# Optimization experiments

Measured on AMD Instinct MI355X. Metric: run time of the kernel, lower is better.

Reference implementation:

```python
import jax, jax.numpy as jnp
import numpy as np

DIM = 1024
HEADS = 16
DIM_HEAD = 64
SEG = 512           # segment_len (+ 0 longterm mem tokens)
PMEM = 16           # num_persist_mem_tokens
THETA = 10000.0
RMS_EPS = 1.1920929e-07  # torch.finfo(float32).eps (nn.RMSNorm default eps=None)


def setup_inputs() -> dict:
    key = jax.random.key(0)
    k0, k1, k2, k3 = jax.random.split(key, 4)
    dim_inner = HEADS * DIM_HEAD
    seq = jax.random.normal(k0, (2, 4096, DIM), jnp.float32)
    norm_w = jnp.ones((DIM,), jnp.float32)
    w_qkv = jax.random.normal(k1, (DIM, 3 * dim_inner), jnp.float32) * (DIM ** -0.5)
    w_out = jax.random.normal(k2, (dim_inner, DIM), jnp.float32) * (dim_inner ** -0.5)
    # nn.Parameter is zeros at init; use small random values for a meaningful test
    pmem = jax.random.normal(k3, (2, HEADS, PMEM, DIM_HEAD), jnp.float32) * 0.02
    return {"seq": seq, "norm_w": norm_w, "w_qkv": w_qkv, "w_out": w_out, "pmem": pmem}


def _rope(x):
    # interleaved (pairwise) rotary over the full head dim, positions 0..n-1 per segment
    n, d = x.shape[-2], x.shape[-1]
    inv_freq = 1.0 / (THETA ** (jnp.arange(0, d, 2, dtype=jnp.float32) / d))
    freqs = jnp.arange(n, dtype=jnp.float32)[:, None] * inv_freq[None, :]  # (n, d/2)
    freqs = jnp.repeat(freqs, 2, axis=-1)                                  # (n, d)
    cos, sin = jnp.cos(freqs), jnp.sin(freqs)
    x1, x2 = x[..., 0::2], x[..., 1::2]
    x_rot = jnp.stack((-x2, x1), axis=-1).reshape(x.shape)
    return x * cos + x_rot * sin


def reference(seq, norm_w, w_qkv, w_out, pmem):
    b, s, d = seq.shape
    w = s // SEG  # seq_len is an exact multiple of segment_len (no pad branch)
    x = seq.reshape(b * w, SEG, d)  # 'b (w n) d -> (b w) n d'
    # RMSNorm
    x = x * jax.lax.rsqrt(jnp.mean(x * x, axis=-1, keepdims=True) + RMS_EPS) * norm_w
    q, k, v = jnp.split(x @ w_qkv, 3, axis=-1)
    sh = lambda t: t.reshape(b * w, SEG, HEADS, DIM_HEAD).transpose(0, 2, 1, 3)  # b n (h d) -> b h n d
    q, k, v = sh(q), sh(k), sh(v)
    orig_v = v
    q, k = _rope(q), _rope(k)
    pmk = jnp.broadcast_to(pmem[0], (b * w, HEADS, PMEM, DIM_HEAD))
    pmv = jnp.broadcast_to(pmem[1], (b * w, HEADS, PMEM, DIM_HEAD))
    k = jnp.concatenate((pmk, k), axis=-2)  # (bw, h, PMEM+SEG, dh)
    v = jnp.concatenate((pmv, v), axis=-2)
    scores = jnp.einsum('bhid,bhjd->bhij', q, k) * (DIM_HEAD ** -0.5)
    i = jnp.arange(SEG)[:, None]
    j = jnp.arange(SEG + PMEM)[None, :]
    mask = (j < PMEM) | ((j - PMEM) <= i)  # persist tokens always visible; causal within segment
    scores = jnp.where(mask, scores, -1e30)
    attn = jax.nn.softmax(scores, axis=-1)
    out = jnp.einsum('bhij,bhjd->bhid', attn, v)
    out = out.transpose(0, 2, 1, 3).reshape(b * w, SEG, HEADS * DIM_HEAD)  # merge heads
    out = (out @ w_out).reshape(b, s, d)  # inverse_segment (no pad to trim)
    return out, orig_v
```

## Files before the change

### kernel.cpp

```cpp
#include <hip/hip_runtime.h>
#include <hip/hip_bf16.h>

#define DIM    1024
#define HEADS  16
#define DH     64
#define SEG    512
#define PMEMN  16
#define TOK    8192
#define NQKV   3072
#define JPAD   544
#define NSH    256
#define VTS    129
#define QKS    136
#define VFS    132

typedef __hip_bfloat16 bf16;
typedef __attribute__((ext_vector_type(8))) short short8;
typedef __attribute__((ext_vector_type(4))) float floatx4;

__device__ __forceinline__ short8 ld_frag(const bf16* p) {
    return *(const short8*)p;
}
__device__ __forceinline__ floatx4 mfma16(short8 a, short8 b, floatx4 c) {
    return __builtin_amdgcn_mfma_f32_16x16x32_bf16(a, b, c, 0, 0, 0);
}
__device__ __forceinline__ void g2lds16(const bf16* g, bf16* l) {
    __builtin_amdgcn_global_load_lds((const __attribute__((address_space(1))) void*)g,
                                     (__attribute__((address_space(3))) void*)l, 16, 0, 0);
}

__global__ void rmsnorm_kernel(const float* __restrict__ x, const float* __restrict__ wgt,
                               bf16* __restrict__ xn) {
    int row = blockIdx.x;
    int tid = threadIdx.x;
    const float4* xr = (const float4*)(x + (long)row * DIM);
    float4 v = xr[tid];
    float ss = v.x * v.x + v.y * v.y + v.z * v.z + v.w * v.w;
    #pragma unroll
    for (int off = 32; off; off >>= 1) ss += __shfl_xor(ss, off);
    __shared__ float red[4];
    if ((tid & 63) == 0) red[tid >> 6] = ss;
    __syncthreads();
    float tot = red[0] + red[1] + red[2] + red[3];
    float sc = rsqrtf(tot * (1.0f / DIM) + 1.1920929e-07f);
    const float4* wr = (const float4*)wgt;
    float4 w4 = wr[tid];
    bf16* o = xn + (long)row * DIM + tid * 4;
    o[0] = __float2bfloat16(v.x * sc * w4.x);
    o[1] = __float2bfloat16(v.y * sc * w4.y);
    o[2] = __float2bfloat16(v.z * sc * w4.z);
    o[3] = __float2bfloat16(v.w * sc * w4.w);
}

__global__ void transpose_w2(const float* __restrict__ wqkv, const float* __restrict__ wout,
                             bf16* __restrict__ wqkvT, bf16* __restrict__ woutT) {
    __shared__ float tile[32][33];
    int bx = blockIdx.x;
    const float* in; bf16* out; int C, c0;
    if (bx < 96) { in = wqkv; out = wqkvT; C = NQKV; c0 = bx * 32; }
    else         { in = wout; out = woutT; C = DIM;  c0 = (bx - 96) * 32; }
    const int R = DIM;
    int r0 = blockIdx.y * 32;
    int tx = threadIdx.x, ty = threadIdx.y;
    #pragma unroll
    for (int i = 0; i < 4; i++)
        tile[ty + i * 8][tx] = in[(long)(r0 + ty + i * 8) * C + c0 + tx];
    __syncthreads();
    #pragma unroll
    for (int i = 0; i < 4; i++)
        out[(long)(c0 + ty + i * 8) * R + r0 + tx] = __float2bfloat16(tile[tx][ty + i * 8]);
}

__global__ __launch_bounds__(256)
void gemm_bt_f(const bf16* __restrict__ A, const bf16* __restrict__ Bt,
               float* __restrict__ C, int M, int N, int K) {
    __shared__ __align__(16) bf16 SMu[128 * 136];
    bf16* As = SMu;
    bf16* Bs = SMu + 128 * 64;
    const int tid = threadIdx.x;
    const int wv = tid >> 6;
    const int lane = tid & 63;
    const int quad = lane >> 4, l15 = lane & 15;
    const int wm = (wv >> 1) * 64, wn = (wv & 1) * 64;
    const int bm = blockIdx.x, bn = blockIdx.y;

    const int srow = tid >> 3;
    const int sgch = (tid & 7) ^ (srow & 7);
    const bf16* Ag = A + (long)(bm * 128 + srow) * K + sgch * 8;
    const bf16* Bg = Bt + (long)(bn * 128 + srow) * K + sgch * 8;
    const long row32 = (long)32 * K;

    const int rx0 = ((0 + quad) ^ (l15 & 7)) * 8;
    const int rx1 = ((4 + quad) ^ (l15 & 7)) * 8;

    floatx4 acc[4][4] = {};

    for (int k0 = 0; k0 < K; k0 += 64) {
        __syncthreads();
        #pragma unroll
        for (int i = 0; i < 4; i++) {
            g2lds16(Ag + i * row32 + k0, As + i * 2048 + tid * 8);
            g2lds16(Bg + i * row32 + k0, Bs + i * 2048 + tid * 8);
        }
        __syncthreads();
        #pragma unroll
        for (int kk = 0; kk < 2; kk++) {
            const int rx = kk ? rx1 : rx0;
            short8 af[4], bfr[4];
            #pragma unroll
            for (int i = 0; i < 4; i++) af[i] = ld_frag(&As[(wm + i * 16 + l15) * 64 + rx]);
            #pragma unroll
            for (int j = 0; j < 4; j++) bfr[j] = ld_frag(&Bs[(wn + j * 16 + l15) * 64 + rx]);
            #pragma unroll
            for (int i = 0; i < 4; i++)
                #pragma unroll
                for (int j = 0; j < 4; j++)
                    acc[i][j] = mfma16(af[i], bfr[j], acc[i][j]);
        }
    }
    float* SMf = (float*)SMu;
    #pragma unroll
    for (int half = 0; half < 2; half++) {
        __syncthreads();
        if ((wv >> 1) == half) {
            #pragma unroll
            for (int i = 0; i < 4; i++)
                #pragma unroll
                for (int j = 0; j < 4; j++)
                    #pragma unroll
                    for (int r = 0; r < 4; r++)
                        SMf[(i * 16 + quad * 4 + r) * VFS + wn + j * 16 + l15] = acc[i][j][r];
        }
        __syncthreads();
        #pragma unroll
        for (int it = 0; it < 8; it++) {
            int cid = it * 256 + tid;
            int rr = cid >> 5, cc = cid & 31;
            float4 v4 = *(const float4*)&SMf[rr * VFS + cc * 4];
            *(float4*)&C[(long)(bm * 128 + half * 64 + rr) * N + bn * 128 + cc * 4] = v4;
        }
    }
}

__global__ __launch_bounds__(256)
void gemm_qkv_ep(const bf16* __restrict__ A, const bf16* __restrict__ Bt,
                 bf16* __restrict__ qbuf, bf16* __restrict__ kpad,
                 bf16* __restrict__ vtpad, float* __restrict__ origv) {
    const int K = DIM, N = NQKV;
    __shared__ __align__(16) bf16 SM[128 * 136];
    bf16* As = SM;
    bf16* Bs = SM + 128 * 64;
    const int tid = threadIdx.x;
    const int wv = tid >> 6;
    const int lane = tid & 63;
    const int quad = lane >> 4, l15 = lane & 15;
    const int wm = (wv >> 1) * 64, wn = (wv & 1) * 64;
    const int bm = blockIdx.x, bn = blockIdx.y;

    const int strow = tid >> 3;
    const int sgch = (tid & 7) ^ (strow & 7);
    const bf16* Ag = A + (long)(bm * 128 + strow) * K + sgch * 8;
    const bf16* Bg = Bt + (long)(bn * 128 + strow) * K + sgch * 8;
    const long row32 = (long)32 * K;

    const int rx0 = ((0 + quad) ^ (l15 & 7)) * 8;
    const int rx1 = ((4 + quad) ^ (l15 & 7)) * 8;

    floatx4 acc[4][4] = {};

    for (int k0 = 0; k0 < K; k0 += 64) {
        __syncthreads();
        #pragma unroll
        for (int i = 0; i < 4; i++) {
            g2lds16(Ag + i * row32 + k0, As + i * 2048 + tid * 8);
            g2lds16(Bg + i * row32 + k0, Bs + i * 2048 + tid * 8);
        }
        __syncthreads();
        #pragma unroll
        for (int kk = 0; kk < 2; kk++) {
            const int rx = kk ? rx1 : rx0;
            short8 af[4], bfr[4];
            #pragma unroll
            for (int i = 0; i < 4; i++) af[i] = ld_frag(&As[(wm + i * 16 + l15) * 64 + rx]);
            #pragma unroll
            for (int j = 0; j < 4; j++) bfr[j] = ld_frag(&Bs[(wn + j * 16 + l15) * 64 + rx]);
            #pragma unroll
            for (int i = 0; i < 4; i++)
                #pragma unroll
                for (int j = 0; j < 4; j++)
                    acc[i][j] = mfma16(af[i], bfr[j], acc[i][j]);
        }
    }

    const int tok0 = bm * 128;
    const int seg = tok0 >> 9;
    const int s0 = tok0 & 511;

    if (bn < 16) {
        const bool isq = (bn < 8);
        __syncthreads();
        #pragma unroll
        for (int j = 0; j < 4; j++) {
            int col = wn + j * 16 + l15;
            int dcol = (bn * 128 + col) & 1023;
            int dh = dcol & 63;
            int pr = dh >> 1;
            float invf = __expf(-(float)pr * (9.210340371976184f / 32.0f));
            const bool odd = dh & 1;
            #pragma unroll
            for (int i = 0; i < 4; i++)
                #pragma unroll
                for (int r = 0; r < 4; r++) {
                    int sl = s0 + wm + i * 16 + quad * 4 + r;
                    float sn, cs;
                    __sincosf((float)sl * invf, &sn, &cs);
                    float v = acc[i][j][r];
                    float px = __shfl_xor(v, 1);
                    float y = odd ? (v * cs + px * sn) : (v * cs - px * sn);
                    if (isq) y *= 0.125f;
                    SM[(wm + i * 16 + quad * 4 + r) * QKS + col] = __float2bfloat16(y);
                }
        }
        __syncthreads();
        #pragma unroll
        for (int it = 0; it < 8; it++) {
            int cid = it * 256 + tid;
            int rr = cid >> 4, cc = cid & 15;
            short8 pk = *(const short8*)&SM[rr * QKS + cc * 8];
            if (isq) {
                *(short8*)&qbuf[(long)(tok0 + rr) * DIM + bn * 128 + cc * 8] = pk;
            } else {
                int lc = cc * 8;
                int h = ((bn - 8) * 128 + lc) >> 6;
                int dh = lc & 63;
                *(short8*)&kpad[(((long)(seg * 16 + h) * JPAD) + PMEMN + s0 + rr) * DH + dh] = pk;
            }
        }
    } else {
        const int vq = bn - 16;
        const int h0 = vq * 2;
        float* SMf = (float*)SM;
        #pragma unroll
        for (int half = 0; half < 2; half++) {
            __syncthreads();
            if ((wv >> 1) == half) {
                #pragma unroll
                for (int i = 0; i < 4; i++)
                    #pragma unroll
                    for (int j = 0; j < 4; j++)
                        #pragma unroll
                        for (int r = 0; r < 4; r++)
                            SMf[(i * 16 + quad * 4 + r) * VFS + wn + j * 16 + l15] = acc[i][j][r];
            }
            __syncthreads();
            #pragma unroll
            for (int it = 0; it < 8; it++) {
                int cid = it * 256 + tid;
                int rr = cid >> 5, cc = cid & 31;
                int h = h0 + (cc >> 4), dh = (cc * 4) & 63;
                float4 v4 = *(const float4*)&SMf[rr * VFS + cc * 4];
                int sl = s0 + half * 64 + rr;
                *(float4*)&origv[((long)(seg * 16 + h) * SEG + sl) * DH + dh] = v4;
            }
        }
        __syncthreads();
        #pragma unroll
        for (int i = 0; i < 4; i++)
            #pragma unroll
            for (int j = 0; j < 4; j++)
                #pragma unroll
                for (int r = 0; r < 4; r++)
                    SM[(wm + i * 16 + quad * 4 + r) * VTS + wn + j * 16 + l15] =
                        __float2bfloat16(acc[i][j][r]);
        __syncthreads();
        #pragma unroll
        for (int it = 0; it < 8; it++) {
            int cid = it * 256 + tid;
            int orow = cid >> 4;
            int tch = cid & 15;
            int vcol = vq * 128 + orow;
            int h = vcol >> 6, dh = vcol & 63;
            short8 pk;
            #pragma unroll
            for (int k = 0; k < 8; k++) {
                bf16 t = SM[(tch * 8 + k) * VTS + orow];
                pk[k] = __builtin_bit_cast(short, t);
            }
            *(short8*)&vtpad[(((long)(seg * 16 + h) * DH + dh) * JPAD) + PMEMN + s0 + tch * 8] = pk;
        }
    }
}

__global__ void fill_pmem_pad(const float* __restrict__ pmem, bf16* __restrict__ kpad,
                              bf16* __restrict__ vtpad) {
    int gid = blockIdx.x * 256 + threadIdx.x;
    int dh = gid & 63, j = (gid >> 6) & 15, sh = gid >> 10;
    int h = sh & 15;
    float kv = pmem[((0 * HEADS + h) * PMEMN + j) * DH + dh];
    float vv = pmem[((1 * HEADS + h) * PMEMN + j) * DH + dh];
    kpad[((long)sh * JPAD + j) * DH + dh] = __float2bfloat16(kv);
    vtpad[((long)sh * DH + dh) * JPAD + j] = __float2bfloat16(vv);
    kpad[((long)sh * JPAD + PMEMN + SEG + j) * DH + dh] = __float2bfloat16(0.0f);
    vtpad[((long)sh * DH + dh) * JPAD + PMEMN + SEG + j] = __float2bfloat16(0.0f);
}

__global__ __launch_bounds__(256, 3)
void flash_attn(const bf16* __restrict__ qbuf, const bf16* __restrict__ kpad,
                const bf16* __restrict__ vtpad, bf16* __restrict__ attn_out) {
    const int bid = blockIdx.x;
    const int sh = bid & (NSH - 1);
    const int qblk = bid >> 8;
    const int wv = threadIdx.x >> 6;
    const int lane = threadIdx.x & 63;
    const int quad = lane >> 4, l15 = lane & 15;
    const int qr0 = qblk * 128 + wv * 32;
    const int bw = sh >> 4, h = sh & 15;

    __shared__ __align__(16) short pbuf[4][32 * 32];
    short* pb = pbuf[wv];

    const bf16* qr_g0 = qbuf + (long)(bw * SEG + qr0 + l15) * DIM + h * DH;
    const bf16* qr_g1 = qbuf + (long)(bw * SEG + qr0 + 16 + l15) * DIM + h * DH;
    short8 aq[2][2] = {{ld_frag(qr_g0 + quad * 8), ld_frag(qr_g0 + 32 + quad * 8)},
                       {ld_frag(qr_g1 + quad * 8), ld_frag(qr_g1 + 32 + quad * 8)}};

    const short bf16one = (short)0x3F80;
    short8 onesB;
    #pragma unroll
    for (int i = 0; i < 8; i++) onesB[i] = (l15 == 0) ? bf16one : (short)0;

    float mrow[2][4];
    floatx4 o[2][4] = {};
    floatx4 lac[2] = {};
    #pragma unroll
    for (int g = 0; g < 2; g++)
        #pragma unroll
        for (int r = 0; r < 4; r++) mrow[g][r] = -1e30f;

    const bf16* kb = kpad + (long)sh * JPAD * DH;
    const bf16* vbp = vtpad + (long)sh * DH * JPAD;

    const int ntiles = (qr0 + 47) / 32 + 1;

    short8 kf[4];
    {
        const bf16* kr0 = kb + (long)l15 * DH;
        const bf16* kr1 = kb + (long)(16 + l15) * DH;
        kf[0] = ld_frag(kr0 + quad * 8);  kf[1] = ld_frag(kr0 + 32 + quad * 8);
        kf[2] = ld_frag(kr1 + quad * 8);  kf[3] = ld_frag(kr1 + 32 + quad * 8);
    }

    for (int jt = 0; jt < ntiles; ++jt) {
        const int j0 = jt * 32;
        short8 bv[4];
        #pragma unroll
        for (int n = 0; n < 4; n++)
            bv[n] = ld_frag(vbp + (long)(n * 16 + l15) * JPAD + j0 + quad * 8);

        floatx4 sc[2][2];
        #pragma unroll
        for (int g = 0; g < 2; g++) {
            sc[g][0] = mfma16(aq[g][1], kf[1], mfma16(aq[g][0], kf[0], floatx4{}));
            sc[g][1] = mfma16(aq[g][1], kf[3], mfma16(aq[g][0], kf[2], floatx4{}));
        }
        {
            const int jn = (jt + 1 < ntiles) ? j0 + 32 : j0;
            const bf16* kr0 = kb + (long)(jn + l15) * DH;
            const bf16* kr1 = kb + (long)(jn + 16 + l15) * DH;
            kf[0] = ld_frag(kr0 + quad * 8);  kf[1] = ld_frag(kr0 + 32 + quad * 8);
            kf[2] = ld_frag(kr1 + quad * 8);  kf[3] = ld_frag(kr1 + 32 + quad * 8);
        }

        float alpha[2][4];
        #pragma unroll
        for (int g = 0; g < 2; g++) {
            #pragma unroll
            for (int r = 0; r < 4; r++) {
                int qi = qr0 + g * 16 + quad * 4 + r;
                int ja = j0 + l15;
                int jb = j0 + 16 + l15;
                float va  = ((ja < PMEMN) || (ja - PMEMN <= qi)) ? sc[g][0][r] : -1e30f;
                float vb2 = ((jb < PMEMN) || (jb - PMEMN <= qi)) ? sc[g][1][r] : -1e30f;
                float rm = fmaxf(va, vb2);
                #pragma unroll
                for (int off = 1; off < 16; off <<= 1) rm = fmaxf(rm, __shfl_xor(rm, off));
                float mn = fmaxf(mrow[g][r], rm);
                alpha[g][r] = __expf(mrow[g][r] - mn);
                mrow[g][r] = mn;
                float p0 = __expf(va - mn);
                float p1 = __expf(vb2 - mn);
                pb[(g * 16 + quad * 4 + r) * 32 + l15]      = __builtin_bit_cast(short, __float2bfloat16(p0));
                pb[(g * 16 + quad * 4 + r) * 32 + 16 + l15] = __builtin_bit_cast(short, __float2bfloat16(p1));
            }
        }
        __asm__ volatile("" ::: "memory");
        short8 pa0, pa1;
        __builtin_memcpy(&pa0, &pb[l15 * 32 + quad * 8], 16);
        __builtin_memcpy(&pa1, &pb[(16 + l15) * 32 + quad * 8], 16);
        __asm__ volatile("" ::: "memory");
        #pragma unroll
        for (int r = 0; r < 4; r++) { lac[0][r] *= alpha[0][r]; lac[1][r] *= alpha[1][r]; }
        lac[0] = mfma16(pa0, onesB, lac[0]);
        lac[1] = mfma16(pa1, onesB, lac[1]);
        #pragma unroll
        for (int n = 0; n < 4; n++) {
            #pragma unroll
            for (int r = 0; r < 4; r++) { o[0][n][r] *= alpha[0][r]; o[1][n][r] *= alpha[1][r]; }
            o[0][n] = mfma16(pa0, bv[n], o[0][n]);
            o[1][n] = mfma16(pa1, bv[n], o[1][n]);
        }
    }
    #pragma unroll
    for (int g = 0; g < 2; g++) {
        bf16* orow = attn_out + (long)(bw * SEG + qr0 + g * 16 + quad * 4) * DIM + h * DH;
        #pragma unroll
        for (int r = 0; r < 4; r++) {
            float lsum = __shfl(lac[g][r], (lane & 48));
            float inv = 1.0f / lsum;
            #pragma unroll
            for (int n = 0; n < 4; n++)
                orow[(long)r * DIM + n * 16 + l15] = __float2bfloat16(o[g][n][r] * inv);
        }
    }
}

extern "C" void kernel_launch(void* const* d_in, const int* in_sizes, int n_in,
                              void* d_out, int out_size, void* d_ws, size_t ws_size,
                              hipStream_t stream) {
    const float* seq    = (const float*)d_in[0];
    const float* norm_w = (const float*)d_in[1];
    const float* w_qkv  = (const float*)d_in[2];
    const float* w_out  = (const float*)d_in[3];
    const float* pmem   = (const float*)d_in[4];
    float* out   = (float*)d_out;
    float* origv = out + (long)TOK * DIM;

    char* p = (char*)d_ws;
    bf16* xn     = (bf16*)p; p += (long)TOK * DIM * 2;
    bf16* wqkvT  = (bf16*)p; p += (long)NQKV * DIM * 2;
    bf16* woutT  = (bf16*)p; p += (long)DIM * DIM * 2;
    bf16* qbuf   = (bf16*)p; p += (long)TOK * DIM * 2;
    bf16* kpadb  = (bf16*)p; p += (long)NSH * JPAD * DH * 2;
    bf16* vtpadb = (bf16*)p; p += (long)NSH * DH * JPAD * 2;
    bf16* attno  = xn;

    rmsnorm_kernel<<<TOK, 256, 0, stream>>>(seq, norm_w, xn);
    transpose_w2<<<dim3(128, 32), dim3(32, 8), 0, stream>>>(w_qkv, w_out, wqkvT, woutT);
    fill_pmem_pad<<<(NSH * PMEMN * DH) / 256, 256, 0, stream>>>(pmem, kpadb, vtpadb);
    gemm_qkv_ep<<<dim3(TOK / 128, NQKV / 128), 256, 0, stream>>>(xn, wqkvT, qbuf, kpadb, vtpadb, origv);
    flash_attn<<<4 * NSH, 256, 0, stream>>>(qbuf, kpadb, vtpadb, attno);
    gemm_bt_f<<<dim3(TOK / 128, DIM / 128), 256, 0, stream>>>(attno, woutT, out, TOK, DIM, DIM);
}
```

Before: 241.6 us.

## Rewrite QKV GEMM as 256x256 tile, 8-wave, double-buffered pipelined kernel

```diff
diff --git a/kernel.cpp b/kernel.cpp
--- a/kernel.cpp
+++ b/kernel.cpp
@@ -11,8 +11,9 @@
 #define JPAD   544
 #define NSH    256
 #define VTS    129
-#define QKS    136
-#define VFS    132
+#define QK2    264
+#define VF2    260
+#define VT2    257
 
 typedef __hip_bfloat16 bf16;
 typedef __attribute__((ext_vector_type(8))) short short8;
@@ -24,6 +25,8 @@
 __device__ __forceinline__ floatx4 mfma16(short8 a, short8 b, floatx4 c) {
     return __builtin_amdgcn_mfma_f32_16x16x32_bf16(a, b, c, 0, 0, 0);
 }
+__device__ __forceinline__ void st_out(bf16* p, float v) { *p = __float2bfloat16(v); }
+__device__ __forceinline__ void st_out(float* p, float v) { *p = v; }
 __device__ __forceinline__ void g2lds16(const bf16* g, bf16* l) {
     __builtin_amdgcn_global_load_lds((const __attribute__((address_space(1))) void*)g,
                                      (__attribute__((address_space(3))) void*)l, 16, 0, 0);
@@ -129,164 +132,210 @@
                 for (int j = 0; j < 4; j++)
                     #pragma unroll
                     for (int r = 0; r < 4; r++)
-                        SMf[(i * 16 + quad * 4 + r) * VFS + wn + j * 16 + l15] = acc[i][j][r];
+                        SMf[(i * 16 + quad * 4 + r) * 132 + wn + j * 16 + l15] = acc[i][j][r];
         }
         __syncthreads();
         #pragma unroll
         for (int it = 0; it < 8; it++) {
             int cid = it * 256 + tid;
             int rr = cid >> 5, cc = cid & 31;
-            float4 v4 = *(const float4*)&SMf[rr * VFS + cc * 4];
+            float4 v4 = *(const float4*)&SMf[rr * 132 + cc * 4];
             *(float4*)&C[(long)(bm * 128 + half * 64 + rr) * N + bn * 128 + cc * 4] = v4;
         }
     }
 }
 
-__global__ __launch_bounds__(256)
+__global__ __launch_bounds__(512, 2)
 void gemm_qkv_ep(const bf16* __restrict__ A, const bf16* __restrict__ Bt,
                  bf16* __restrict__ qbuf, bf16* __restrict__ kpad,
                  bf16* __restrict__ vtpad, float* __restrict__ origv) {
-    const int K = DIM, N = NQKV;
-    __shared__ __align__(16) bf16 SM[128 * 136];
-    bf16* As = SM;
-    bf16* Bs = SM + 128 * 64;
+    __shared__ __align__(16) bf16 SMEM[65536];
     const int tid = threadIdx.x;
     const int wv = tid >> 6;
     const int lane = tid & 63;
     const int quad = lane >> 4, l15 = lane & 15;
-    const int wm = (wv >> 1) * 64, wn = (wv & 1) * 64;
+    const int qrow = wv >> 1;
+    const int qcol = wv & 1;
     const int bm = blockIdx.x, bn = blockIdx.y;
 
-    const int strow = tid >> 3;
-    const int sgch = (tid & 7) ^ (strow & 7);
-    const bf16* Ag = A + (long)(bm * 128 + strow) * K + sgch * 8;
-    const bf16* Bg = Bt + (long)(bn * 128 + strow) * K + sgch * 8;
-    const long row32 = (long)32 * K;
-
-    const int rx0 = ((0 + quad) ^ (l15 & 7)) * 8;
-    const int rx1 = ((4 + quad) ^ (l15 & 7)) * 8;
-
-    floatx4 acc[4][4] = {};
-
-    for (int k0 = 0; k0 < K; k0 += 64) {
-        __syncthreads();
-        #pragma unroll
-        for (int i = 0; i < 4; i++) {
-            g2lds16(Ag + i * row32 + k0, As + i * 2048 + tid * 8);
-            g2lds16(Bg + i * row32 + k0, Bs + i * 2048 + tid * 8);
-        }
-        __syncthreads();
-        #pragma unroll
-        for (int kk = 0; kk < 2; kk++) {
-            const int rx = kk ? rx1 : rx0;
-            short8 af[4], bfr[4];
-            #pragma unroll
-            for (int i = 0; i < 4; i++) af[i] = ld_frag(&As[(wm + i * 16 + l15) * 64 + rx]);
-            #pragma unroll
-            for (int j = 0; j < 4; j++) bfr[j] = ld_frag(&Bs[(wn + j * 16 + l15) * 64 + rx]);
-            #pragma unroll
-            for (int i = 0; i < 4; i++)
-                #pragma unroll
-                for (int j = 0; j < 4; j++)
-                    acc[i][j] = mfma16(af[i], bfr[j], acc[i][j]);
-        }
-    }
-
-    const int tok0 = bm * 128;
+    const int rowt = tid >> 3;
+    const int sgch = (tid & 7) ^ (rowt & 7);
+    const bf16* Asrc = A  + (long)(bm * 256 + rowt) * DIM + sgch * 8;
+    const bf16* Bsrc = Bt + (long)(bn * 256 + rowt) * DIM + sgch * 8;
+
+#define STG_A(buf, h, kt) do { \
+        g2lds16(Asrc + (long)((h) * 128 +  0) * DIM + (kt) * 64, SMEM + (buf) * 16384 + ((h) * 128 +  0) * 64 + tid * 8); \
+        g2lds16(Asrc + (long)((h) * 128 + 64) * DIM + (kt) * 64, SMEM + (buf) * 16384 + ((h) * 128 + 64) * 64 + tid * 8); \
+    } while (0)
+#define STG_B(buf, h, kt) do { \
+        g2lds16(Bsrc + (long)((h) * 128 +  0) * DIM + (kt) * 64, SMEM + 32768 + (buf) * 16384 + ((h) * 128 +  0) * 64 + tid * 8); \
+        g2lds16(Bsrc + (long)((h) * 128 + 64) * DIM + (kt) * 64, SMEM + 32768 + (buf) * 16384 + ((h) * 128 + 64) * 64 + tid * 8); \
+    } while (0)
+
+    floatx4 acc[2][2][2][4] = {};
+
+#define PHASE(CUR, MH, NH, STGBLK, DOWAIT) do { \
+        short8 af[2][2], bfv[2][4]; \
+        _Pragma("unroll") \
+        for (int m = 0; m < 2; m++) \
+            _Pragma("unroll") \
+            for (int kk = 0; kk < 2; kk++) \
+                af[kk][m] = ld_frag(&SMEM[(CUR) * 16384 + ((MH) * 128 + qrow * 32 + m * 16 + l15) * 64 + ((kk * 4 + quad) ^ (l15 & 7)) * 8]); \
+        _Pragma("unroll") \
+        for (int n = 0; n < 4; n++) \
+            _Pragma("unroll") \
+            for (int kk = 0; kk < 2; kk++) \
+                bfv[kk][n] = ld_frag(&SMEM[32768 + (CUR) * 16384 + ((NH) * 128 + qcol * 64 + n * 16 + l15) * 64 + ((kk * 4 + quad) ^ (l15 & 7)) * 8]); \
+        STGBLK; \
+        __builtin_amdgcn_s_barrier(); \
+        asm volatile("s_waitcnt lgkmcnt(0)" ::: "memory"); \
+        __builtin_amdgcn_sched_barrier(0); \
+        __builtin_amdgcn_s_setprio(1); \
+        _Pragma("unroll") \
+        for (int m = 0; m < 2; m++) \
+            _Pragma("unroll") \
+            for (int n = 0; n < 4; n++) { \
+                acc[MH][NH][m][n] = mfma16(af[0][m], bfv[0][n], acc[MH][NH][m][n]); \
+                acc[MH][NH][m][n] = mfma16(af[1][m], bfv[1][n], acc[MH][NH][m][n]); \
+            } \
+        __builtin_amdgcn_s_setprio(0); \
+        if (DOWAIT) { asm volatile("s_waitcnt vmcnt(4)" ::: "memory"); } \
+        __builtin_amdgcn_s_barrier(); \
+    } while (0)
+
+    STG_A(0, 0, 0); STG_B(0, 0, 0); STG_B(0, 1, 0); STG_A(0, 1, 0);
+    asm volatile("s_waitcnt vmcnt(4)" ::: "memory");
+    __builtin_amdgcn_s_barrier();
+
+    for (int kt2 = 0; kt2 < 16; kt2 += 2) {
+        {
+            const int kn = kt2 + 1;
+            PHASE(0, 0, 0, STG_A(1, 0, kn), 1);
+            PHASE(0, 0, 1, STG_B(1, 0, kn), 1);
+            PHASE(0, 1, 0, STG_B(1, 1, kn), 0);
+            PHASE(0, 1, 1, STG_A(1, 1, kn), 1);
+        }
+        {
+            const int kn = (kt2 + 2 < 16) ? kt2 + 2 : 15;
+            PHASE(1, 0, 0, STG_A(0, 0, kn), 1);
+            PHASE(1, 0, 1, STG_B(0, 0, kn), 1);
+            PHASE(1, 1, 0, STG_B(0, 1, kn), 0);
+            PHASE(1, 1, 1, STG_A(0, 1, kn), 1);
+        }
+    }
+    asm volatile("s_waitcnt vmcnt(0)" ::: "memory");
+    __builtin_amdgcn_s_barrier();
+#undef PHASE
+#undef STG_A
+#undef STG_B
+
+    const int tok0 = bm * 256;
     const int seg = tok0 >> 9;
     const int s0 = tok0 & 511;
 
-    if (bn < 16) {
-        const bool isq = (bn < 8);
-        __syncthreads();
-        #pragma unroll
-        for (int j = 0; j < 4; j++) {
-            int col = wn + j * 16 + l15;
-            int dcol = (bn * 128 + col) & 1023;
-            int dh = dcol & 63;
-            int pr = dh >> 1;
-            float invf = __expf(-(float)pr * (9.210340371976184f / 32.0f));
-            const bool odd = dh & 1;
-            #pragma unroll
-            for (int i = 0; i < 4; i++)
-                #pragma unroll
-                for (int r = 0; r < 4; r++) {
-                    int sl = s0 + wm + i * 16 + quad * 4 + r;
-                    float sn, cs;
-                    __sincosf((float)sl * invf, &sn, &cs);
-                    float v = acc[i][j][r];
-                    float px = __shfl_xor(v, 1);
-                    float y = odd ? (v * cs + px * sn) : (v * cs - px * sn);
-                    if (isq) y *= 0.125f;
-                    SM[(wm + i * 16 + quad * 4 + r) * QKS + col] = __float2bfloat16(y);
+    if (bn < 8) {
+        const bool isq = (bn < 4);
+        const int cb = (bn & 3) * 256;
+        #pragma unroll
+        for (int mh = 0; mh < 2; mh++) {
+            __syncthreads();
+            #pragma unroll
+            for (int nh = 0; nh < 2; nh++)
+                #pragma unroll
+                for (int n = 0; n < 4; n++) {
+                    int col = nh * 128 + qcol * 64 + n * 16 + l15;
+                    int dcol = cb + col;
+                    int dh = dcol & 63;
+                    int pr = dh >> 1;
+                    float invf = __expf(-(float)pr * (9.210340371976184f / 32.0f));
+                    const bool odd = dh & 1;
+                    #pragma unroll
+                    for (int m = 0; m < 2; m++)
+                        #pragma unroll
+                        for (int r = 0; r < 4; r++) {
+                            int lrow = qrow * 32 + m * 16 + quad * 4 + r;
+                            int sl = s0 + mh * 128 + lrow;
+                            float sn, cs;
+                            __sincosf((float)sl * invf, &sn, &cs);
+                            float v = acc[mh][nh][m][n][r];
+                            float px = __shfl_xor(v, 1);
+                            float y = odd ? (v * cs + px * sn) : (v * cs - px * sn);
+                            if (isq) y *= 0.125f;
+                            SMEM[lrow * QK2 + col] = __float2bfloat16(y);
+                        }
                 }
-        }
-        __syncthreads();
-        #pragma unroll
-        for (int it = 0; it < 8; it++) {
-            int cid = it * 256 + tid;
-            int rr = cid >> 4, cc = cid & 15;
-            short8 pk = *(const short8*)&SM[rr * QKS + cc * 8];
-            if (isq) {
-                *(short8*)&qbuf[(long)(tok0 + rr) * DIM + bn * 128 + cc * 8] = pk;
-            } else {
-                int lc = cc * 8;
-                int h = ((bn - 8) * 128 + lc) >> 6;
-                int dh = lc & 63;
-                *(short8*)&kpad[(((long)(seg * 16 + h) * JPAD) + PMEMN + s0 + rr) * DH + dh] = pk;
+            __syncthreads();
+            #pragma unroll
+            for (int it = 0; it < 8; it++) {
+                int cid = it * 512 + tid;
+                int rr = cid >> 5, cc = cid & 31;
+                short8 pk = *(const short8*)&SMEM[rr * QK2 + cc * 8];
+                if (isq) {
+                    *(short8*)&qbuf[(long)(tok0 + mh * 128 + rr) * DIM + cb + cc * 8] = pk;
+                } else {
+                    int dcol = cb + cc * 8;
+                    int h = dcol >> 6, dh = dcol & 63;
+                    *(short8*)&kpad[(((long)(seg * 16 + h) * JPAD) + PMEMN + s0 + mh * 128 + rr) * DH + dh] = pk;
+                }
             }
         }
     } else {
-        const int vq = bn - 16;
-        const int h0 = vq * 2;
-        float* SMf = (float*)SM;
-        #pragma unroll
-        for (int half = 0; half < 2; half++) {
+        const int vb = (bn - 8) * 256;
+        float* SMf = (float*)SMEM;
+        #pragma unroll
+        for (int qt = 0; qt < 4; qt++) {
             __syncthreads();
-            if ((wv >> 1) == half) {
-                #pragma unroll
-                for (int i = 0; i < 4; i++)
+            if ((qrow >> 1) == (qt & 1)) {
+                #pragma unroll
+                for (int nh = 0; nh < 2; nh++)
                     #pragma unroll
-                    for (int j = 0; j < 4; j++)
+                    for (int m = 0; m < 2; m++)
+                        #pragma unroll
+                        for (int n = 0; n < 4; n++)
+                            #pragma unroll
+                            for (int r = 0; r < 4; r++)
+                                SMf[((qrow & 1) * 32 + m * 16 + quad * 4 + r) * VF2 + nh * 128 + qcol * 64 + n * 16 + l15] =
+                                    acc[qt >> 1][nh][m][n][r];
+            }
+            __syncthreads();
+            #pragma unroll
+            for (int it = 0; it < 8; it++) {
+                int cid = it * 512 + tid;
+                int rr = cid >> 6, cc = cid & 63;
+                float4 v4 = *(const float4*)&SMf[rr * VF2 + cc * 4];
+                int sl = s0 + qt * 64 + rr;
+                int vcol = vb + cc * 4;
+                int h = vcol >> 6, dh = vcol & 63;
+                *(float4*)&origv[((long)(seg * 16 + h) * SEG + sl) * DH + dh] = v4;
+            }
+        }
+        #pragma unroll
+        for (int hf = 0; hf < 2; hf++) {
+            __syncthreads();
+            #pragma unroll
+            for (int nh = 0; nh < 2; nh++)
+                #pragma unroll
+                for (int m = 0; m < 2; m++)
+                    #pragma unroll
+                    for (int n = 0; n < 4; n++)
                         #pragma unroll
                         for (int r = 0; r < 4; r++)
-                            SMf[(i * 16 + quad * 4 + r) * VFS + wn + j * 16 + l15] = acc[i][j][r];
+                            SMEM[(qrow * 32 + m * 16 + quad * 4 + r) * VT2 + nh * 128 + qcol * 64 + n * 16 + l15] =
+                                __float2bfloat16(acc[hf][nh][m][n][r]);
+            __syncthreads();
+            #pragma unroll
+            for (int it = 0; it < 8; it++) {
+                int cid = it * 512 + tid;
+                int orow = cid >> 4;
+                int tch = cid & 15;
+                int vcol = vb + orow;
+                int h = vcol >> 6, dh = vcol & 63;
+                short8 pk;
+                #pragma unroll
+                for (int k = 0; k < 8; k++)
+                    pk[k] = __builtin_bit_cast(short, SMEM[(tch * 8 + k) * VT2 + orow]);
+                *(short8*)&vtpad[(((long)(seg * 16 + h) * DH + dh) * JPAD) + PMEMN + s0 + hf * 128 + tch * 8] = pk;
             }
-            __syncthreads();
-            #pragma unroll
-            for (int it = 0; it < 8; it++) {
-                int cid = it * 256 + tid;
-                int rr = cid >> 5, cc = cid & 31;
-                int h = h0 + (cc >> 4), dh = (cc * 4) & 63;
-                float4 v4 = *(const float4*)&SMf[rr * VFS + cc * 4];
-                int sl = s0 + half * 64 + rr;
-                *(float4*)&origv[((long)(seg * 16 + h) * SEG + sl) * DH + dh] = v4;
-            }
-        }
-        __syncthreads();
-        #pragma unroll
-        for (int i = 0; i < 4; i++)
-            #pragma unroll
-            for (int j = 0; j < 4; j++)
-                #pragma unroll
-                for (int r = 0; r < 4; r++)
-                    SM[(wm + i * 16 + quad * 4 + r) * VTS + wn + j * 16 + l15] =
-                        __float2bfloat16(acc[i][j][r]);
-        __syncthreads();
-        #pragma unroll
-        for (int it = 0; it < 8; it++) {
-            int cid = it * 256 + tid;
-            int orow = cid >> 4;
-            int tch = cid & 15;
-            int vcol = vq * 128 + orow;
-            int h = vcol >> 6, dh = vcol & 63;
-            short8 pk;
-            #pragma unroll
-            for (int k = 0; k < 8; k++) {
-                bf16 t = SM[(tch * 8 + k) * VTS + orow];
-                pk[k] = __builtin_bit_cast(short, t);
-            }
-            *(short8*)&vtpad[(((long)(seg * 16 + h) * DH + dh) * JPAD) + PMEMN + s0 + tch * 8] = pk;
         }
     }
 }
@@ -447,7 +496,7 @@
     rmsnorm_kernel<<<TOK, 256, 0, stream>>>(seq, norm_w, xn);
     transpose_w2<<<dim3(128, 32), dim3(32, 8), 0, stream>>>(w_qkv, w_out, wqkvT, woutT);
     fill_pmem_pad<<<(NSH * PMEMN * DH) / 256, 256, 0, stream>>>(pmem, kpadb, vtpadb);
-    gemm_qkv_ep<<<dim3(TOK / 128, NQKV / 128), 256, 0, stream>>>(xn, wqkvT, qbuf, kpadb, vtpadb, origv);
+    gemm_qkv_ep<<<dim3(TOK / 256, NQKV / 256), 512, 0, stream>>>(xn, wqkvT, qbuf, kpadb, vtpadb, origv);
     flash_attn<<<4 * NSH, 256, 0, stream>>>(qbuf, kpadb, vtpadb, attno);
     gemm_bt_f<<<dim3(TOK / 128, DIM / 128), 256, 0, stream>>>(attno, woutT, out, TOK, DIM, DIM);
 }
```

Result: slower. 253.2 us (+4.8%).

## Move Q rotary into attention kernel, fold Q scale into weights, remap block order

Applied to the files above, without the earlier changes.

```diff
diff --git a/kernel.cpp b/kernel.cpp
--- a/kernel.cpp
+++ b/kernel.cpp
@@ -56,8 +56,8 @@
                              bf16* __restrict__ wqkvT, bf16* __restrict__ woutT) {
     __shared__ float tile[32][33];
     int bx = blockIdx.x;
-    const float* in; bf16* out; int C, c0;
-    if (bx < 96) { in = wqkv; out = wqkvT; C = NQKV; c0 = bx * 32; }
+    const float* in; bf16* out; int C, c0; float scl = 1.0f;
+    if (bx < 96) { in = wqkv; out = wqkvT; C = NQKV; c0 = bx * 32; if (bx < 32) scl = 0.125f; }
     else         { in = wout; out = woutT; C = DIM;  c0 = (bx - 96) * 32; }
     const int R = DIM;
     int r0 = blockIdx.y * 32;
@@ -68,7 +68,7 @@
     __syncthreads();
     #pragma unroll
     for (int i = 0; i < 4; i++)
-        out[(long)(c0 + ty + i * 8) * R + r0 + tx] = __float2bfloat16(tile[tx][ty + i * 8]);
+        out[(long)(c0 + ty + i * 8) * R + r0 + tx] = __float2bfloat16(tile[tx][ty + i * 8] * scl);
 }
 
 __global__ __launch_bounds__(256)
@@ -129,14 +129,14 @@
                 for (int j = 0; j < 4; j++)
                     #pragma unroll
                     for (int r = 0; r < 4; r++)
-                        SMf[(i * 16 + quad * 4 + r) * VFS + wn + j * 16 + l15] = acc[i][j][r];
+                        SMf[(i * 16 + quad * 4 + r) * 132 + wn + j * 16 + l15] = acc[i][j][r];
         }
         __syncthreads();
         #pragma unroll
         for (int it = 0; it < 8; it++) {
             int cid = it * 256 + tid;
             int rr = cid >> 5, cc = cid & 31;
-            float4 v4 = *(const float4*)&SMf[rr * VFS + cc * 4];
+            float4 v4 = *(const float4*)&SMf[rr * 132 + cc * 4];
             *(float4*)&C[(long)(bm * 128 + half * 64 + rr) * N + bn * 128 + cc * 4] = v4;
         }
     }
@@ -199,27 +199,37 @@
     if (bn < 16) {
         const bool isq = (bn < 8);
         __syncthreads();
-        #pragma unroll
-        for (int j = 0; j < 4; j++) {
-            int col = wn + j * 16 + l15;
-            int dcol = (bn * 128 + col) & 1023;
-            int dh = dcol & 63;
-            int pr = dh >> 1;
-            float invf = __expf(-(float)pr * (9.210340371976184f / 32.0f));
-            const bool odd = dh & 1;
-            #pragma unroll
-            for (int i = 0; i < 4; i++)
-                #pragma unroll
-                for (int r = 0; r < 4; r++) {
-                    int sl = s0 + wm + i * 16 + quad * 4 + r;
-                    float sn, cs;
-                    __sincosf((float)sl * invf, &sn, &cs);
-                    float v = acc[i][j][r];
-                    float px = __shfl_xor(v, 1);
-                    float y = odd ? (v * cs + px * sn) : (v * cs - px * sn);
-                    if (isq) y *= 0.125f;
-                    SM[(wm + i * 16 + quad * 4 + r) * QKS + col] = __float2bfloat16(y);
-                }
+        if (isq) {
+            #pragma unroll
+            for (int j = 0; j < 4; j++)
+                #pragma unroll
+                for (int i = 0; i < 4; i++)
+                    #pragma unroll
+                    for (int r = 0; r < 4; r++)
+                        SM[(wm + i * 16 + quad * 4 + r) * QKS + wn + j * 16 + l15] =
+                            __float2bfloat16(acc[i][j][r]);
+        } else {
+            #pragma unroll
+            for (int j = 0; j < 4; j++) {
+                int col = wn + j * 16 + l15;
+                int dcol = (bn * 128 + col) & 1023;
+                int dh = dcol & 63;
+                int pr = dh >> 1;
+                float invf = __expf(-(float)pr * (9.210340371976184f / 32.0f));
+                const bool odd = dh & 1;
+                #pragma unroll
+                for (int i = 0; i < 4; i++)
+                    #pragma unroll
+                    for (int r = 0; r < 4; r++) {
+                        int sl = s0 + wm + i * 16 + quad * 4 + r;
+                        float sn, cs;
+                        __sincosf((float)sl * invf, &sn, &cs);
+                        float v = acc[i][j][r];
+                        float px = __shfl_xor(v, 1);
+                        float y = odd ? (v * cs + px * sn) : (v * cs - px * sn);
+                        SM[(wm + i * 16 + quad * 4 + r) * QKS + col] = __float2bfloat16(y);
+                    }
+            }
         }
         __syncthreads();
         #pragma unroll
@@ -308,8 +318,8 @@
 void flash_attn(const bf16* __restrict__ qbuf, const bf16* __restrict__ kpad,
                 const bf16* __restrict__ vtpad, bf16* __restrict__ attn_out) {
     const int bid = blockIdx.x;
-    const int sh = bid & (NSH - 1);
-    const int qblk = bid >> 8;
+    const int sh = bid >> 2;
+    const int qblk = bid & 3;
     const int wv = threadIdx.x >> 6;
     const int lane = threadIdx.x & 63;
     const int quad = lane >> 4, l15 = lane & 15;
@@ -323,6 +333,25 @@
     const bf16* qr_g1 = qbuf + (long)(bw * SEG + qr0 + 16 + l15) * DIM + h * DH;
     short8 aq[2][2] = {{ld_frag(qr_g0 + quad * 8), ld_frag(qr_g0 + 32 + quad * 8)},
                        {ld_frag(qr_g1 + quad * 8), ld_frag(qr_g1 + 32 + quad * 8)}};
+
+    #pragma unroll
+    for (int g = 0; g < 2; g++) {
+        float slf = (float)(qr0 + g * 16 + l15);
+        #pragma unroll
+        for (int f = 0; f < 2; f++) {
+            #pragma unroll
+            for (int p = 0; p < 4; p++) {
+                int pr = ((f * 32 + quad * 8) >> 1) + p;
+                float invf = __expf(-(float)pr * (9.210340371976184f / 32.0f));
+                float sn, cs;
+                __sincosf(slf * invf, &sn, &cs);
+                float x0 = __builtin_bit_cast(float, (unsigned)(unsigned short)aq[g][f][2 * p] << 16);
+                float x1 = __builtin_bit_cast(float, (unsigned)(unsigned short)aq[g][f][2 * p + 1] << 16);
+                aq[g][f][2 * p]     = __builtin_bit_cast(short, __float2bfloat16(x0 * cs - x1 * sn));
+                aq[g][f][2 * p + 1] = __builtin_bit_cast(short, __float2bfloat16(x1 * cs + x0 * sn));
+            }
+        }
+    }
 
     const short bf16one = (short)0x3F80;
     short8 onesB;
```

Result: slower. 254.9 us (+5.5%).
